# Kernel optimization log

Measured on AMD Instinct MI355X. Metric: run time of the kernel, lower is better.

## Reference

```python
import jax, jax.numpy as jnp
import numpy as np

B, T, I, D, O = 256, 512, 64, 512, 128
LN_EPS = 1e-5


def setup_inputs() -> dict:
    key = jax.random.key(0)
    ks = jax.random.split(key, 4)
    x = jax.random.normal(ks[0], (B, T, I), dtype=jnp.float32)
    W_in = jax.random.normal(ks[1], (D, I), dtype=jnp.float32) * (1.0 / np.sqrt(I))
    b_in = jnp.zeros((D,), dtype=jnp.float32)
    gamma = jnp.ones((D,), dtype=jnp.float32)
    beta = jnp.zeros((D,), dtype=jnp.float32)
    W_out = jax.random.normal(ks[2], (O, D), dtype=jnp.float32) * (1.0 / np.sqrt(D))
    b_out = jnp.zeros((O,), dtype=jnp.float32)
    context_strength = jnp.float32(0.2)
    return {"x": x, "W_in": W_in, "b_in": b_in, "gamma": gamma, "beta": beta,
            "W_out": W_out, "b_out": b_out, "context_strength": context_strength}


def reference(x, W_in, b_in, gamma, beta, W_out, b_out, context_strength):
    # memory_ring slot 0 is the only one ever read/written, so context_read at
    # step t is simply state_update from step t-1 (zeros at t=0).
    b, t, _ = x.shape
    d = W_in.shape[0]
    # Precompute all input embeddings in one GEMM: [B,T,D]
    e = jnp.tanh(jnp.einsum('bti,di->btd', x, W_in) + b_in)
    scale = jax.nn.sigmoid(context_strength)

    def layer_norm(s):
        mu = jnp.mean(s, axis=-1, keepdims=True)
        var = jnp.mean((s - mu) ** 2, axis=-1, keepdims=True)
        return (s - mu) * jax.lax.rsqrt(var + LN_EPS) * gamma + beta

    def step(carry, e_t):
        s_prev, h_prev = carry  # state_update_{t-1}, hidden_{t-1}
        s = jnp.tanh(e_t + scale * s_prev + h_prev)
        h = layer_norm(s)
        return (s, h), None

    init = (jnp.zeros((b, d), dtype=x.dtype), jnp.zeros((b, d), dtype=x.dtype))
    (_, h_final), _ = jax.lax.scan(step, init, jnp.swapaxes(e, 0, 1))  # scan over T
    logits = h_final @ W_out.T + b_out  # [B,O]
    return logits
```

## Files before the change

### kernel.cpp

```cpp
#include <hip/hip_runtime.h>

#define BB 256
#define TT 512
#define II 64
#define DD 512
#define OO 128
#define LN_EPS 1e-5f
#define XS_STRIDE 68
#define WS_STRIDE 132

__device__ __forceinline__ float fast_tanh(float x) {
    float e = __expf(2.0f * x);
    return 1.0f - 2.0f / (e + 1.0f);
}

__global__ __launch_bounds__(256, 2)
void embed_kernel(const float* __restrict__ x,
                  const float* __restrict__ W_in,
                  const float* __restrict__ b_in,
                  float* __restrict__ E,
                  int t0, int CT)
{
    __shared__ float xs[II][XS_STRIDE];
    __shared__ float ws[II][WS_STRIDE];

    const int tiles_per_b = CT >> 6;
    const int bx   = blockIdx.x;
    const int b    = bx / tiles_per_b;
    const int tau0 = (bx - b * tiles_per_b) << 6;
    const int d0   = blockIdx.y << 7;
    const int tid  = threadIdx.x;

    {
        const int r0 = tid >> 4;
        const int c4 = tid & 15;
        #pragma unroll
        for (int rr = 0; rr < 8; ++rr) {
            const int row = r0 + (rr << 4);
            const float4 wv = *(const float4*)(W_in + ((size_t)(d0 + row)) * II + c4 * 4);
            ws[c4 * 4 + 0][row] = wv.x; ws[c4 * 4 + 1][row] = wv.y;
            ws[c4 * 4 + 2][row] = wv.z; ws[c4 * 4 + 3][row] = wv.w;
            if (rr < 4) {
                const float4 xv = *(const float4*)(x + ((size_t)(b * TT + t0 + tau0 + row)) * II + c4 * 4);
                xs[c4 * 4 + 0][row] = xv.x; xs[c4 * 4 + 1][row] = xv.y;
                xs[c4 * 4 + 2][row] = xv.z; xs[c4 * 4 + 3][row] = xv.w;
            }
        }
    }
    __syncthreads();

    const int tn = tid & 15;
    const int td = tid >> 4;

    float acc[4][8];
    #pragma unroll
    for (int j = 0; j < 4; ++j)
        #pragma unroll
        for (int k = 0; k < 8; ++k) acc[j][k] = 0.0f;

    #pragma unroll 4
    for (int i = 0; i < II; ++i) {
        const float4 xv = *(const float4*)&xs[i][tn * 4];
        const float4 wa = *(const float4*)&ws[i][td * 8];
        const float4 wb = *(const float4*)&ws[i][td * 8 + 4];
        #pragma unroll
        for (int j = 0; j < 4; ++j) {
            const float xj = (j == 0) ? xv.x : (j == 1) ? xv.y : (j == 2) ? xv.z : xv.w;
            acc[j][0] = fmaf(xj, wa.x, acc[j][0]);
            acc[j][1] = fmaf(xj, wa.y, acc[j][1]);
            acc[j][2] = fmaf(xj, wa.z, acc[j][2]);
            acc[j][3] = fmaf(xj, wa.w, acc[j][3]);
            acc[j][4] = fmaf(xj, wb.x, acc[j][4]);
            acc[j][5] = fmaf(xj, wb.y, acc[j][5]);
            acc[j][6] = fmaf(xj, wb.z, acc[j][6]);
            acc[j][7] = fmaf(xj, wb.w, acc[j][7]);
        }
    }

    const int dg = d0 + td * 8;
    const float4 bv0 = *(const float4*)(b_in + dg);
    const float4 bv1 = *(const float4*)(b_in + dg + 4);
    #pragma unroll
    for (int j = 0; j < 4; ++j) {
        const int n = tau0 + tn * 4 + j;
        float4 e0, e1;
        e0.x = fast_tanh(acc[j][0] + bv0.x);
        e0.y = fast_tanh(acc[j][1] + bv0.y);
        e0.z = fast_tanh(acc[j][2] + bv0.z);
        e0.w = fast_tanh(acc[j][3] + bv0.w);
        e1.x = fast_tanh(acc[j][4] + bv1.x);
        e1.y = fast_tanh(acc[j][5] + bv1.y);
        e1.z = fast_tanh(acc[j][6] + bv1.z);
        e1.w = fast_tanh(acc[j][7] + bv1.w);
        float* dst = E + ((size_t)(b * CT + n)) * DD + dg;
        *(float4*)(dst)     = e0;
        *(float4*)(dst + 4) = e1;
    }
}

__global__ __launch_bounds__(256)
void recur_kernel(const float* __restrict__ E,
                  const float* __restrict__ gamma,
                  const float* __restrict__ beta,
                  const float* __restrict__ W_out,
                  const float* __restrict__ b_out,
                  const float* __restrict__ cs,
                  float* __restrict__ s_state,
                  float* __restrict__ h_state,
                  float* __restrict__ out,
                  int CT, int is_first, int is_last)
{
    const int b    = blockIdx.x;
    const int tid  = threadIdx.x;
    const int wave = tid >> 6;
    const int lane = tid & 63;
    const int d2   = tid << 1;

    __shared__ __align__(16) float red[2][4][2];
    __shared__ float h_lds[DD];

    const float2 g  = *(const float2*)(gamma + d2);
    const float2 bt = *(const float2*)(beta  + d2);
    const float scale = 1.0f / (1.0f + __expf(-cs[0]));

    float2 sp, hp;
    if (is_first) { sp.x = sp.y = 0.0f; hp = sp; }
    else {
        sp = *(const float2*)(s_state + (size_t)b * DD + d2);
        hp = *(const float2*)(h_state + (size_t)b * DD + d2);
    }

    const float* Eb = E + (size_t)b * CT * DD;
    float2 e0 = *(const float2*)(Eb + d2);
    float2 e1 = *(const float2*)(Eb + DD + d2);

    #pragma unroll 1
    for (int tau = 0; tau < CT; ++tau) {
        const int tpre = (tau + 2 < CT) ? tau + 2 : CT - 1;
        const float2 e2 = *(const float2*)(Eb + (size_t)tpre * DD + d2);

        float2 s;
        s.x = fast_tanh(e0.x + scale * sp.x + hp.x);
        s.y = fast_tanh(e0.y + scale * sp.y + hp.y);

        float r0 = s.x + s.y;
        float r1 = s.x * s.x + s.y * s.y;
        #pragma unroll
        for (int m = 32; m >= 1; m >>= 1) {
            r0 += __shfl_xor(r0, m, 64);
            r1 += __shfl_xor(r1, m, 64);
        }

        const int p = tau & 1;
        if (lane == 0) { red[p][wave][0] = r0; red[p][wave][1] = r1; }
        __syncthreads();

        const float4 ra = *(const float4*)&red[p][0][0];
        const float4 rb = *(const float4*)&red[p][2][0];
        const float sum   = (ra.x + ra.z) + (rb.x + rb.z);
        const float sumsq = (ra.y + ra.w) + (rb.y + rb.w);

        const float mu   = sum * (1.0f / DD);
        const float var  = sumsq * (1.0f / DD) - mu * mu;
        const float rstd = rsqrtf(var + LN_EPS);

        hp.x = (s.x - mu) * rstd * g.x + bt.x;
        hp.y = (s.y - mu) * rstd * g.y + bt.y;
        sp = s;
        e0 = e1;
        e1 = e2;
    }

    if (!is_last) {
        *(float2*)(s_state + (size_t)b * DD + d2) = sp;
        *(float2*)(h_state + (size_t)b * DD + d2) = hp;
    } else {
        h_lds[d2]     = hp.x;
        h_lds[d2 + 1] = hp.y;
        __syncthreads();

        const int dbase = lane * 8;
        float hreg[8];
        #pragma unroll
        for (int k = 0; k < 8; ++k) hreg[k] = h_lds[dbase + k];

        for (int oo = 0; oo < 32; ++oo) {
            const int o = wave * 32 + oo;
            const float* wo = W_out + (size_t)o * DD + dbase;
            float pacc = 0.f;
            #pragma unroll
            for (int k = 0; k < 8; ++k) pacc = fmaf(wo[k], hreg[k], pacc);
            #pragma unroll
            for (int m = 32; m >= 1; m >>= 1) pacc += __shfl_xor(pacc, m, 64);
            if (lane == 0) out[(size_t)b * OO + o] = pacc + b_out[o];
        }
    }
}

extern "C" void kernel_launch(void* const* d_in, const int* in_sizes, int n_in,
                              void* d_out, int out_size, void* d_ws, size_t ws_size,
                              hipStream_t stream) {
    const float* x      = (const float*)d_in[0];
    const float* W_in   = (const float*)d_in[1];
    const float* b_in   = (const float*)d_in[2];
    const float* gamma  = (const float*)d_in[3];
    const float* beta   = (const float*)d_in[4];
    const float* W_out  = (const float*)d_in[5];
    const float* b_out  = (const float*)d_in[6];
    const float* cs     = (const float*)d_in[7];
    float* out = (float*)d_out;

    const size_t state_bytes = (size_t)BB * DD * sizeof(float);
    int CT = TT;
    while (CT > 64 &&
           (size_t)BB * CT * DD * sizeof(float) + 2 * state_bytes > ws_size) {
        CT >>= 1;
    }
    float* E       = (float*)d_ws;
    float* s_state = (float*)((char*)d_ws + (size_t)BB * CT * DD * sizeof(float));
    float* h_state = s_state + (size_t)BB * DD;

    const int nchunks = TT / CT;
    for (int c = 0; c < nchunks; ++c) {
        dim3 g1(BB * (CT >> 6), DD >> 7);
        embed_kernel<<<g1, 256, 0, stream>>>(x, W_in, b_in, E, c * CT, CT);
        recur_kernel<<<BB, 256, 0, stream>>>(E, gamma, beta, W_out, b_out, cs,
                                             s_state, h_state, out, CT,
                                             (c == 0) ? 1 : 0,
                                             (c == nchunks - 1) ? 1 : 0);
    }
}
```

Measured before the change: 472.9 us.

## Fuse input embedding GEMM into recurrent kernel, computing e_t per step in registers

Removes the separate embedding kernel and its E buffer in workspace. Each thread now keeps its two rows of W_in in registers (128 floats) and computes the next step's embedding dot products while the LayerNorm reduction is in flight, with x rows double-buffered in LDS. This removes the large write and re-read of E through global memory and the chunked multi-launch. In exchange it adds 128 FMAs per thread per step on the serial critical path and heavy register pressure, with only 256 blocks available to fill the GPU.

New measurement: 553.0 us. 1.17x slower.

```diff
diff --git a/kernel.cpp b/kernel.cpp
--- a/kernel.cpp
+++ b/kernel.cpp
@@ -6,109 +6,22 @@
 #define DD 512
 #define OO 128
 #define LN_EPS 1e-5f
-#define XS_STRIDE 68
-#define WS_STRIDE 132
 
 __device__ __forceinline__ float fast_tanh(float x) {
     float e = __expf(2.0f * x);
     return 1.0f - 2.0f / (e + 1.0f);
 }
 
-__global__ __launch_bounds__(256, 2)
-void embed_kernel(const float* __restrict__ x,
+__global__ __launch_bounds__(256)
+void fused_kernel(const float* __restrict__ x,
                   const float* __restrict__ W_in,
                   const float* __restrict__ b_in,
-                  float* __restrict__ E,
-                  int t0, int CT)
-{
-    __shared__ float xs[II][XS_STRIDE];
-    __shared__ float ws[II][WS_STRIDE];
-
-    const int tiles_per_b = CT >> 6;
-    const int bx   = blockIdx.x;
-    const int b    = bx / tiles_per_b;
-    const int tau0 = (bx - b * tiles_per_b) << 6;
-    const int d0   = blockIdx.y << 7;
-    const int tid  = threadIdx.x;
-
-    {
-        const int r0 = tid >> 4;
-        const int c4 = tid & 15;
-        #pragma unroll
-        for (int rr = 0; rr < 8; ++rr) {
-            const int row = r0 + (rr << 4);
-            const float4 wv = *(const float4*)(W_in + ((size_t)(d0 + row)) * II + c4 * 4);
-            ws[c4 * 4 + 0][row] = wv.x; ws[c4 * 4 + 1][row] = wv.y;
-            ws[c4 * 4 + 2][row] = wv.z; ws[c4 * 4 + 3][row] = wv.w;
-            if (rr < 4) {
-                const float4 xv = *(const float4*)(x + ((size_t)(b * TT + t0 + tau0 + row)) * II + c4 * 4);
-                xs[c4 * 4 + 0][row] = xv.x; xs[c4 * 4 + 1][row] = xv.y;
-                xs[c4 * 4 + 2][row] = xv.z; xs[c4 * 4 + 3][row] = xv.w;
-            }
-        }
-    }
-    __syncthreads();
-
-    const int tn = tid & 15;
-    const int td = tid >> 4;
-
-    float acc[4][8];
-    #pragma unroll
-    for (int j = 0; j < 4; ++j)
-        #pragma unroll
-        for (int k = 0; k < 8; ++k) acc[j][k] = 0.0f;
-
-    #pragma unroll 4
-    for (int i = 0; i < II; ++i) {
-        const float4 xv = *(const float4*)&xs[i][tn * 4];
-        const float4 wa = *(const float4*)&ws[i][td * 8];
-        const float4 wb = *(const float4*)&ws[i][td * 8 + 4];
-        #pragma unroll
-        for (int j = 0; j < 4; ++j) {
-            const float xj = (j == 0) ? xv.x : (j == 1) ? xv.y : (j == 2) ? xv.z : xv.w;
-            acc[j][0] = fmaf(xj, wa.x, acc[j][0]);
-            acc[j][1] = fmaf(xj, wa.y, acc[j][1]);
-            acc[j][2] = fmaf(xj, wa.z, acc[j][2]);
-            acc[j][3] = fmaf(xj, wa.w, acc[j][3]);
-            acc[j][4] = fmaf(xj, wb.x, acc[j][4]);
-            acc[j][5] = fmaf(xj, wb.y, acc[j][5]);
-            acc[j][6] = fmaf(xj, wb.z, acc[j][6]);
-            acc[j][7] = fmaf(xj, wb.w, acc[j][7]);
-        }
-    }
-
-    const int dg = d0 + td * 8;
-    const float4 bv0 = *(const float4*)(b_in + dg);
-    const float4 bv1 = *(const float4*)(b_in + dg + 4);
-    #pragma unroll
-    for (int j = 0; j < 4; ++j) {
-        const int n = tau0 + tn * 4 + j;
-        float4 e0, e1;
-        e0.x = fast_tanh(acc[j][0] + bv0.x);
-        e0.y = fast_tanh(acc[j][1] + bv0.y);
-        e0.z = fast_tanh(acc[j][2] + bv0.z);
-        e0.w = fast_tanh(acc[j][3] + bv0.w);
-        e1.x = fast_tanh(acc[j][4] + bv1.x);
-        e1.y = fast_tanh(acc[j][5] + bv1.y);
-        e1.z = fast_tanh(acc[j][6] + bv1.z);
-        e1.w = fast_tanh(acc[j][7] + bv1.w);
-        float* dst = E + ((size_t)(b * CT + n)) * DD + dg;
-        *(float4*)(dst)     = e0;
-        *(float4*)(dst + 4) = e1;
-    }
-}
-
-__global__ __launch_bounds__(256)
-void recur_kernel(const float* __restrict__ E,
                   const float* __restrict__ gamma,
                   const float* __restrict__ beta,
                   const float* __restrict__ W_out,
                   const float* __restrict__ b_out,
                   const float* __restrict__ cs,
-                  float* __restrict__ s_state,
-                  float* __restrict__ h_state,
-                  float* __restrict__ out,
-                  int CT, int is_first, int is_last)
+                  float* __restrict__ out)
 {
     const int b    = blockIdx.x;
     const int tid  = threadIdx.x;
@@ -116,32 +29,59 @@
     const int lane = tid & 63;
     const int d2   = tid << 1;
 
+    __shared__ __align__(16) float4 xrow[2][16];
     __shared__ __align__(16) float red[2][4][2];
     __shared__ float h_lds[DD];
 
-    const float2 g  = *(const float2*)(gamma + d2);
-    const float2 bt = *(const float2*)(beta  + d2);
+    float4 wA[16], wB[16];
+    {
+        const float* wrA = W_in + (size_t)d2 * II;
+        const float* wrB = W_in + (size_t)(d2 + 1) * II;
+        #pragma unroll
+        for (int k = 0; k < 16; ++k) {
+            wA[k] = *(const float4*)(wrA + k * 4);
+            wB[k] = *(const float4*)(wrB + k * 4);
+        }
+    }
+    const float2 bin = *(const float2*)(b_in + d2);
+    const float2 g   = *(const float2*)(gamma + d2);
+    const float2 bt  = *(const float2*)(beta  + d2);
     const float scale = 1.0f / (1.0f + __expf(-cs[0]));
 
+    const float* xb = x + (size_t)b * TT * II;
+
+    float4 xg;
+    if (tid < 16) {
+        xrow[0][tid] = *(const float4*)(xb + (size_t)0 * II + tid * 4);
+        xrow[1][tid] = *(const float4*)(xb + (size_t)1 * II + tid * 4);
+        xg           = *(const float4*)(xb + (size_t)2 * II + tid * 4);
+    }
+    __syncthreads();
+
+    float2 ecur;
+    {
+        float ax = 0.0f, ay = 0.0f;
+        #pragma unroll
+        for (int k = 0; k < 16; ++k) {
+            const float4 xv = xrow[0][k];
+            ax = fmaf(xv.x, wA[k].x, ax); ax = fmaf(xv.y, wA[k].y, ax);
+            ax = fmaf(xv.z, wA[k].z, ax); ax = fmaf(xv.w, wA[k].w, ax);
+            ay = fmaf(xv.x, wB[k].x, ay); ay = fmaf(xv.y, wB[k].y, ay);
+            ay = fmaf(xv.z, wB[k].z, ay); ay = fmaf(xv.w, wB[k].w, ay);
+        }
+        ecur.x = fast_tanh(ax + bin.x);
+        ecur.y = fast_tanh(ay + bin.y);
+    }
+    __syncthreads();
+
     float2 sp, hp;
-    if (is_first) { sp.x = sp.y = 0.0f; hp = sp; }
-    else {
-        sp = *(const float2*)(s_state + (size_t)b * DD + d2);
-        hp = *(const float2*)(h_state + (size_t)b * DD + d2);
-    }
-
-    const float* Eb = E + (size_t)b * CT * DD;
-    float2 e0 = *(const float2*)(Eb + d2);
-    float2 e1 = *(const float2*)(Eb + DD + d2);
+    sp.x = sp.y = 0.0f; hp = sp;
 
     #pragma unroll 1
-    for (int tau = 0; tau < CT; ++tau) {
-        const int tpre = (tau + 2 < CT) ? tau + 2 : CT - 1;
-        const float2 e2 = *(const float2*)(Eb + (size_t)tpre * DD + d2);
-
+    for (int t = 0; t < TT; ++t) {
         float2 s;
-        s.x = fast_tanh(e0.x + scale * sp.x + hp.x);
-        s.y = fast_tanh(e0.y + scale * sp.y + hp.y);
+        s.x = fast_tanh(ecur.x + scale * sp.x + hp.x);
+        s.y = fast_tanh(ecur.y + scale * sp.y + hp.y);
 
         float r0 = s.x + s.y;
         float r1 = s.x * s.x + s.y * s.y;
@@ -151,8 +91,30 @@
             r1 += __shfl_xor(r1, m, 64);
         }
 
-        const int p = tau & 1;
+        float2 en;
+        {
+            float ax = 0.0f, ay = 0.0f;
+            const float4* xr = xrow[(t + 1) & 1];
+            #pragma unroll
+            for (int k = 0; k < 16; ++k) {
+                const float4 xv = xr[k];
+                ax = fmaf(xv.x, wA[k].x, ax); ax = fmaf(xv.y, wA[k].y, ax);
+                ax = fmaf(xv.z, wA[k].z, ax); ax = fmaf(xv.w, wA[k].w, ax);
+                ay = fmaf(xv.x, wB[k].x, ay); ay = fmaf(xv.y, wB[k].y, ay);
+                ay = fmaf(xv.z, wB[k].z, ay); ay = fmaf(xv.w, wB[k].w, ay);
+            }
+            en.x = fast_tanh(ax + bin.x);
+            en.y = fast_tanh(ay + bin.y);
+        }
+
+        const int p = t & 1;
         if (lane == 0) { red[p][wave][0] = r0; red[p][wave][1] = r1; }
+
+        if (tid < 16) {
+            xrow[t & 1][tid] = xg;
+            const int tld = (t + 3 < TT) ? (t + 3) : (TT - 1);
+            xg = *(const float4*)(xb + (size_t)tld * II + tid * 4);
+        }
         __syncthreads();
 
         const float4 ra = *(const float4*)&red[p][0][0];
@@ -167,33 +129,27 @@
         hp.x = (s.x - mu) * rstd * g.x + bt.x;
         hp.y = (s.y - mu) * rstd * g.y + bt.y;
         sp = s;
-        e0 = e1;
-        e1 = e2;
+        ecur = en;
     }
 
-    if (!is_last) {
-        *(float2*)(s_state + (size_t)b * DD + d2) = sp;
-        *(float2*)(h_state + (size_t)b * DD + d2) = hp;
-    } else {
-        h_lds[d2]     = hp.x;
-        h_lds[d2 + 1] = hp.y;
-        __syncthreads();
+    h_lds[d2]     = hp.x;
+    h_lds[d2 + 1] = hp.y;
+    __syncthreads();
 
-        const int dbase = lane * 8;
-        float hreg[8];
+    const int dbase = lane * 8;
+    float hreg[8];
+    #pragma unroll
+    for (int k = 0; k < 8; ++k) hreg[k] = h_lds[dbase + k];
+
+    for (int oo = 0; oo < 32; ++oo) {
+        const int o = wave * 32 + oo;
+        const float* wo = W_out + (size_t)o * DD + dbase;
+        float pacc = 0.f;
         #pragma unroll
-        for (int k = 0; k < 8; ++k) hreg[k] = h_lds[dbase + k];
-
-        for (int oo = 0; oo < 32; ++oo) {
-            const int o = wave * 32 + oo;
-            const float* wo = W_out + (size_t)o * DD + dbase;
-            float pacc = 0.f;
-            #pragma unroll
-            for (int k = 0; k < 8; ++k) pacc = fmaf(wo[k], hreg[k], pacc);
-            #pragma unroll
-            for (int m = 32; m >= 1; m >>= 1) pacc += __shfl_xor(pacc, m, 64);
-            if (lane == 0) out[(size_t)b * OO + o] = pacc + b_out[o];
-        }
+        for (int k = 0; k < 8; ++k) pacc = fmaf(wo[k], hreg[k], pacc);
+        #pragma unroll
+        for (int m = 32; m >= 1; m >>= 1) pacc += __shfl_xor(pacc, m, 64);
+        if (lane == 0) out[(size_t)b * OO + o] = pacc + b_out[o];
     }
 }
 
@@ -210,23 +166,8 @@
     const float* cs     = (const float*)d_in[7];
     float* out = (float*)d_out;
 
-    const size_t state_bytes = (size_t)BB * DD * sizeof(float);
-    int CT = TT;
-    while (CT > 64 &&
-           (size_t)BB * CT * DD * sizeof(float) + 2 * state_bytes > ws_size) {
-        CT >>= 1;
-    }
-    float* E       = (float*)d_ws;
-    float* s_state = (float*)((char*)d_ws + (size_t)BB * CT * DD * sizeof(float));
-    float* h_state = s_state + (size_t)BB * DD;
+    (void)d_ws; (void)ws_size;
 
-    const int nchunks = TT / CT;
-    for (int c = 0; c < nchunks; ++c) {
-        dim3 g1(BB * (CT >> 6), DD >> 7);
-        embed_kernel<<<g1, 256, 0, stream>>>(x, W_in, b_in, E, c * CT, CT);
-        recur_kernel<<<BB, 256, 0, stream>>>(E, gamma, beta, W_out, b_out, cs,
-                                             s_state, h_state, out, CT,
-                                             (c == 0) ? 1 : 0,
-                                             (c == nchunks - 1) ? 1 : 0);
-    }
+    fused_kernel<<<BB, 256, 0, stream>>>(x, W_in, b_in, gamma, beta,
+                                         W_out, b_out, cs, out);
 }
```
